# Performance work log

Measured on AMD Instinct MI355X. Metric: run time of the kernel, lower is better.

Reference implementation:

```python
import jax, jax.numpy as jnp
import numpy as np

B, NPTS = 2, 60000
NX, NY = 256, 256
PCR0, PCR1 = -32.0, -32.0
PS0, PS1 = 0.25, 0.25
MAXPP = 32      # max points per pillar
MAXP = 12000    # max pillars
C = 64          # lidar_channels
SENT = NX * NY  # sentinel pillar id (> any valid id)
NEG = -1e9
EPS = 1e-5


def setup_inputs():
    key = jax.random.key(0)
    ks = jax.random.split(key, 16)
    xy = jax.random.uniform(ks[0], (B, NPTS, 2), minval=-34.0, maxval=34.0)
    z = jax.random.uniform(ks[1], (B, NPTS, 1), minval=-3.0, maxval=1.0)
    ir = jax.random.uniform(ks[2], (B, NPTS, 2))
    pts = jnp.concatenate([xy, z, ir], axis=-1).astype(jnp.float32)
    mask = jax.random.uniform(ks[3], (B, NPTS)) < 0.98

    def lin(k, i, o):
        return (jax.random.normal(k, (i, o)) / np.sqrt(i)).astype(jnp.float32)

    inp = {"lidar_points": pts, "lidar_mask": mask,
           "w1": lin(ks[4], 10, 64), "b1": 0.01 * jax.random.normal(ks[5], (64,), jnp.float32),
           "g1": jnp.ones(64, jnp.float32), "be1": jnp.zeros(64, jnp.float32),
           "w2": lin(ks[6], 64, 64), "b2": 0.01 * jax.random.normal(ks[7], (64,), jnp.float32),
           "g2": jnp.ones(64, jnp.float32), "be2": jnp.zeros(64, jnp.float32)}
    for i, n in enumerate(["1", "2", "3"]):
        inp["cw" + n] = (jax.random.normal(ks[8 + i], (64, 64, 3, 3)) / np.sqrt(64 * 9)).astype(jnp.float32)
        inp["cb" + n] = 0.01 * jax.random.normal(ks[11 + i], (64,), jnp.float32)
        inp["cg" + n] = jnp.ones(64, jnp.float32)
        inp["cbe" + n] = jnp.zeros(64, jnp.float32)
    return inp


def bn1d(x, g, b):  # training-mode BN over rows (biased var), matches torch BatchNorm1d forward
    m = x.mean(0)
    v = ((x - m) ** 2).mean(0)
    return (x - m) * jax.lax.rsqrt(v + EPS) * g + b


def bn2d(x, g, b):  # training-mode BN over (N,H,W) per channel
    m = x.mean((0, 2, 3), keepdims=True)
    v = ((x - m) ** 2).mean((0, 2, 3), keepdims=True)
    return (x - m) * jax.lax.rsqrt(v + EPS) * g[None, :, None, None] + b[None, :, None, None]


def conv3(x, w, b):
    y = jax.lax.conv_general_dilated(x, w, (1, 1), 'SAME',
                                     dimension_numbers=('NCHW', 'OIHW', 'NCHW'))
    return y + b[None, :, None, None]


def pillarize(pts, msk):
    """pts: (N,5) xyzir, msk: (N,) bool -> padded pillar tensors (fixed shapes)."""
    n = pts.shape[0]
    ix = jnp.clip(((pts[:, 0] - PCR0) / PS0).astype(jnp.int32), 0, NX - 1)
    iy = jnp.clip(((pts[:, 1] - PCR1) / PS1).astype(jnp.int32), 0, NY - 1)
    pid = jnp.where(msk, iy * NX + ix, SENT)
    # sorted unique ids; keep the first (smallest) MAXP, like torch.unique + truncation
    spid = jnp.sort(pid)
    is_new = jnp.concatenate([jnp.array([True]), spid[1:] != spid[:-1]])
    urank = jnp.cumsum(is_new) - 1
    dest = jnp.where(is_new & (urank < MAXP) & (spid < SENT), urank, MAXP)
    uids = jnp.full((MAXP + 1,), SENT, dtype=pid.dtype).at[dest].set(spid)[:MAXP]  # ascending, SENT-padded
    inv = jnp.clip(jnp.searchsorted(uids, pid), 0, MAXP - 1)
    valid = (uids[inv] == pid) & (pid < SENT)
    # rank of each point within its pillar, in original point order (stable sort)
    seg = jnp.where(valid, inv, MAXP)
    order = jnp.argsort(seg)  # stable
    sseg = seg[order]
    pos = jnp.arange(n)
    first = jnp.concatenate([jnp.array([True]), sseg[1:] != sseg[:-1]])
    start = jax.lax.cummax(jnp.where(first, pos, 0))
    rank = jnp.zeros(n, jnp.int32).at[order].set((pos - start).astype(jnp.int32))
    keep = valid & (rank < MAXPP)  # first MAXPP points per pillar (matches truncation-then-mean)
    seg2 = jnp.where(keep, inv, MAXP)  # dump slot = MAXP
    cnt = jnp.zeros(MAXP + 1, pts.dtype).at[seg2].add(1.0)
    sums = jnp.zeros((MAXP + 1, 3), pts.dtype).at[seg2].add(jnp.where(keep[:, None], pts[:, :3], 0.0))
    mean = sums / jnp.maximum(cnt, 1.0)[:, None]
    ctr = mean[seg2]  # per-point pillar centroid (over kept points)
    gx = PCR0 + ((pid % NX).astype(pts.dtype) + 0.5) * PS0
    gy = PCR1 + ((pid // NX).astype(pts.dtype) + 0.5) * PS1
    aug = jnp.concatenate([pts, pts[:, :3] - ctr, gx[:, None], gy[:, None]], axis=1)  # (N,10)
    rk = jnp.minimum(rank, MAXPP - 1)
    pf = jnp.zeros((MAXP + 1, MAXPP, 10), pts.dtype).at[seg2, rk].set(
        jnp.where(keep[:, None], aug, 0.0))[:MAXP]
    pm = jnp.zeros((MAXP + 1, MAXPP), bool).at[seg2, rk].set(keep)[:MAXP]
    pvalid = uids < SENT
    coords = jnp.where(pvalid[:, None], jnp.stack([uids % NX, uids // NX], axis=-1), 0)
    return pf, pm, coords, pvalid


def pillar_net(pf, pm, w1, b1, g1, be1, w2, b2, g2, be2):
    npil, pp, ci = pf.shape
    x = pf.reshape(npil * pp, ci) @ w1 + b1
    x = jax.nn.relu(bn1d(x, g1, be1))
    x = x @ w2 + b2
    x = jax.nn.relu(bn1d(x, g2, be2))
    x = x.reshape(npil, pp, -1)
    x = jnp.where(pm[:, :, None], x, NEG)
    return x.max(axis=1)  # (npil, C)


def reference(lidar_points, lidar_mask, w1, b1, g1, be1, w2, b2, g2, be2,
              cw1, cb1, cg1, cbe1, cw2, cb2, cg2, cbe2, cw3, cb3, cg3, cbe3):
    pf, pm, coords, pvalid = jax.vmap(pillarize)(lidar_points, lidar_mask)
    # pillar net is applied per batch element in the original loop -> per-sample BN stats
    feat = jax.vmap(lambda a, m: pillar_net(a, m, w1, b1, g1, be1, w2, b2, g2, be2))(pf, pm)
    lin = coords[..., 1] * NX + coords[..., 0]          # (B, MAXP)
    f = jnp.where(pvalid[..., None], feat, 0.0)          # padded pillars contribute nothing
    bev = jax.vmap(lambda l, ff: jnp.zeros((NY * NX, C), ff.dtype).at[l].add(ff))(lin, f)
    bev = bev.reshape(-1, NY, NX, C).transpose(0, 3, 1, 2)  # (B,C,NY,NX)
    x = jax.nn.relu(bn2d(conv3(bev, cw1, cb1), cg1, cbe1))
    x = jax.nn.relu(bn2d(conv3(x, cw2, cb2), cg2, cbe2))
    x = jax.nn.relu(bn2d(conv3(x, cw3, cb3), cg3, cbe3))
    return x
```

## Files before the change

### kernel.cpp

```cpp
#include <hip/hip_runtime.h>

#define NPTS 60000
#define NXG 256
#define NCELL 65536
#define MAXP 12000
#define MAXPP 32
#define NROWS (MAXP*MAXPP)

typedef float f32x32 __attribute__((ext_vector_type(32)));
typedef float f32x4  __attribute__((ext_vector_type(4)));
typedef short s16x8  __attribute__((ext_vector_type(8)));

__device__ __forceinline__ short to_bf16(float f){
  unsigned u = __float_as_uint(f);
  unsigned r = (u + 0x7FFFu + ((u>>16)&1u)) >> 16;
  return (short)r;
}
__device__ __forceinline__ unsigned mapf(float f){
  unsigned u = __float_as_uint(f);
  return (u & 0x80000000u) ? ~u : (u | 0x80000000u);
}
__device__ __forceinline__ float unmapf(unsigned u){
  unsigned b = (u & 0x80000000u) ? (u ^ 0x80000000u) : ~u;
  return __uint_as_float(b);
}

__global__ __launch_bounds__(256) void prep(uint4* __restrict__ p1, size_t n1,
                                            uint4* __restrict__ p2, size_t n2,
                                            const float* __restrict__ w0, const float* __restrict__ w1,
                                            const float* __restrict__ w2, short* __restrict__ wh,
                                            const float* __restrict__ mw1, const float* __restrict__ mw2,
                                            short* __restrict__ w1h, short* __restrict__ w2h,
                                            uint4* __restrict__ fmn, size_t nfmn){
  size_t idx = (size_t)blockIdx.x*256 + threadIdx.x;
  size_t stride = (size_t)gridDim.x*256;
  const uint4 z = make_uint4(0,0,0,0);
  const uint4 ff = make_uint4(0xFFFFFFFFu,0xFFFFFFFFu,0xFFFFFFFFu,0xFFFFFFFFu);
  for (size_t k=idx; k<n1; k+=stride) p1[k]=z;
  for (size_t k=idx; k<n2; k+=stride) p2[k]=z;
  for (size_t k=idx; k<nfmn; k+=stride) fmn[k]=ff;
  for (size_t k=idx; k<3*36864; k+=stride){
    int l = (int)(k / 36864), r = (int)(k - (size_t)l*36864);
    const float* w = (l==0)? w0 : ((l==1)? w1 : w2);
    int ic = r & 63, oc = (r>>6)&63, tap = r>>12;
    wh[k] = to_bf16(w[(oc*64+ic)*9 + tap]);
  }
  for (size_t k=idx; k<2048; k+=stride){
    int kk = (int)(k>>6), oc = (int)(k&63);
    w1h[k] = (kk<10) ? to_bf16(mw1[kk*64+oc]) : (short)0;
  }
  for (size_t k=idx; k<4096; k+=stride)
    w2h[k] = to_bf16(mw2[k]);
}

__global__ void compute_pid(const float* __restrict__ pts, const void* __restrict__ maskp,
                            int* __restrict__ pid, int* __restrict__ pptr,
                            int* __restrict__ ccnt){
  __shared__ int cf32, cbig;
  if (threadIdx.x==0){ cf32=0; cbig=0; }
  __syncthreads();
  {
    int lf=0, lb=0;
    const unsigned* mu = (const unsigned*)maskp;
    for (int k=0;k<4;k++){
      unsigned x = mu[threadIdx.x*4+k];
      if (x==0x3f800000u) lf++;
      else if (x>1u) lb++;
    }
    if (lf) atomicAdd(&cf32, lf);
    if (lb) atomicAdd(&cbig, lb);
  }
  __syncthreads();
  int mode = (cf32>64) ? 2 : ((cbig>0) ? 1 : 0);
  int i = blockIdx.x*blockDim.x + threadIdx.x;
  if (i>=NPTS) return;
  int b = blockIdx.y;
  int gi = b*NPTS+i;
  bool m;
  if (mode==0)      m = ((const int*)maskp)[gi]!=0;
  else if (mode==1) m = ((const unsigned char*)maskp)[gi]!=0;
  else              m = ((const float*)maskp)[gi]!=0.f;
  int cell = -1;
  if (m){
    float x = pts[(size_t)gi*5+0], y = pts[(size_t)gi*5+1];
    int ix = (int)((x - (-32.0f)) / 0.25f);
    ix = ix<0?0:(ix>255?255:ix);
    int iy = (int)((y - (-32.0f)) / 0.25f);
    iy = iy<0?0:(iy>255?255:iy);
    cell = iy*NXG + ix;
    atomicAdd(&ccnt[b*NCELL+cell], 1);
  }
  pid[gi] = cell;
  pptr[gi] = -1;
}

__global__ __launch_bounds__(256) void scan_a(const int* __restrict__ ccnt,
                                              int2* __restrict__ bpart){
  int b = blockIdx.y, blk = blockIdx.x, t = threadIdx.x;
  int4 v = *(const int4*)&ccnt[b*NCELL + blk*1024 + t*4];
  int occ = (v.x>0)+(v.y>0)+(v.z>0)+(v.w>0);
  int cnt = v.x+v.y+v.z+v.w;
  #pragma unroll
  for (int off=32; off>0; off>>=1){
    occ += __shfl_xor(occ, off, 64);
    cnt += __shfl_xor(cnt, off, 64);
  }
  __shared__ int so[4], sc[4];
  int wv = t>>6, lane = t&63;
  if (lane==0){ so[wv]=occ; sc[wv]=cnt; }
  __syncthreads();
  if (t==0) bpart[b*64+blk] = make_int2(so[0]+so[1]+so[2]+so[3], sc[0]+sc[1]+sc[2]+sc[3]);
}

__global__ __launch_bounds__(256) void scan_b(const int* __restrict__ ccnt,
    const int2* __restrict__ bpart,
    int* __restrict__ crank, int* __restrict__ cstart, int* __restrict__ pcell,
    int* __restrict__ misc, int* __restrict__ heavy){
  __shared__ int swo[4], swc[4], sk[4];
  __shared__ int bo_, bc_;
  int b = blockIdx.y, blk = blockIdx.x, t = threadIdx.x;
  int wv = t>>6, lane = t&63;
  if (t < 64){
    int2 p = bpart[b*64+t];
    int po = (t<blk)? p.x : 0;
    int pc = (t<blk)? p.y : 0;
    int to = p.x;
    int tc = p.y;
    #pragma unroll
    for (int off=32; off>0; off>>=1){
      po += __shfl_xor(po, off, 64);
      pc += __shfl_xor(pc, off, 64);
      to += __shfl_xor(to, off, 64);
      tc += __shfl_xor(tc, off, 64);
    }
    if (t==0){
      bo_ = po; bc_ = pc;
      if (blk==0){
        misc[1+b] = (to < MAXP) ? to : MAXP;
        misc[5+b] = tc;
      }
    }
  }
  int4 v = *(const int4*)&ccnt[b*NCELL + blk*1024 + t*4];
  int occ = (v.x>0)+(v.y>0)+(v.z>0)+(v.w>0);
  int cnt = v.x+v.y+v.z+v.w;
  int io = occ, ic = cnt;
  #pragma unroll
  for (int off=1; off<64; off<<=1){
    int ao = __shfl_up(io, off, 64);
    int ac = __shfl_up(ic, off, 64);
    if (lane >= off){ io += ao; ic += ac; }
  }
  if (lane==63){ swo[wv]=io; swc[wv]=ic; }
  __syncthreads();
  int wvo=0, wvc=0;
  #pragma unroll
  for (int w2=0; w2<4; w2++){
    if (w2<wv){ wvo += swo[w2]; wvc += swc[w2]; }
  }
  int eo = bo_ + wvo + io - occ;
  int ec = bc_ + wvc + ic - cnt;
  int kept = 0;
  int cellb = blk*1024 + t*4;
  int vv[4] = {v.x,v.y,v.z,v.w};
  #pragma unroll
  for (int j=0;j<4;j++){
    int c = cellb+j; int val = vv[j];
    if (val>0){
      crank[b*NCELL+c]=eo; cstart[b*NCELL+c]=ec;
      if (eo<MAXP){
        pcell[b*MAXP+eo]=c;
        kept += (val<MAXPP)? val : MAXPP;
        if (val>MAXPP){
          int hi = atomicAdd(&heavy[b],1);
          if (hi<64) heavy[2 + b*64 + hi] = c;
        }
      }
      eo++; ec+=val;
    }
  }
  #pragma unroll
  for (int off=32; off>0; off>>=1) kept += __shfl_xor(kept, off, 64);
  if (lane==0) sk[wv]=kept;
  __syncthreads();
  if (t==0) atomicAdd(&misc[3+b], sk[0]+sk[1]+sk[2]+sk[3]);
}

__global__ void scatter_points(const int* __restrict__ pid, const int* __restrict__ ccnt,
    const int* __restrict__ crank, const int* __restrict__ cstart,
    int* __restrict__ ctmp, int* __restrict__ plist, int* __restrict__ pptr){
  int i = blockIdx.x*blockDim.x + threadIdx.x;
  if (i>=NPTS) return;
  int b = blockIdx.y;
  int gi = b*NPTS+i;
  int cell = pid[gi];
  if (cell<0) return;
  int bc = b*NCELL+cell;
  int pos = cstart[bc] + atomicAdd(&ctmp[bc],1);
  plist[b*NPTS+pos] = i;
  int r = crank[bc];
  if (r>=0 && r<MAXP && ccnt[bc]<=MAXPP) pptr[gi] = r;
}

__global__ void heavy_select(const int* __restrict__ ccnt, const int* __restrict__ crank,
    const int* __restrict__ cstart, const int* __restrict__ plist,
    const int* __restrict__ heavy, int* __restrict__ pptr){
  int b = blockIdx.y;
  int hn = heavy[b]; if (hn>64) hn=64;
  if ((int)blockIdx.x >= hn) return;
  int cell = heavy[2 + b*64 + blockIdx.x];
  int bc = b*NCELL+cell;
  int cnt = ccnt[bc], start = cstart[bc], pr = crank[bc];
  for (int e=threadIdx.x; e<cnt; e+=blockDim.x){
    int pe = plist[b*NPTS+start+e];
    int rank=0;
    for (int k=0;k<cnt;k++) rank += (plist[b*NPTS+start+k] < pe);
    if (rank<MAXPP) pptr[b*NPTS+pe] = pr;
  }
}

__global__ __launch_bounds__(256) void gather_cpts(const float* __restrict__ pts,
    const int* __restrict__ pid, const int* __restrict__ pptr,
    const int* __restrict__ plist, const int* __restrict__ misc,
    float* __restrict__ cpts, float* __restrict__ psum){
  int pos = blockIdx.x*256 + threadIdx.x;
  int b = blockIdx.y;
  if (pos >= misc[5+b]) return;
  int i = plist[b*NPTS+pos];
  int gi = b*NPTS+i;
  const float* qp = &pts[(size_t)gi*5];
  float x=qp[0], y=qp[1], z=qp[2], i1=qp[3], i2=qp[4];
  int cell = pid[gi];
  int rid = pptr[gi];
  float gx = -32.0f + ((float)(cell&255)+0.5f)*0.25f;
  float gy = -32.0f + ((float)(cell>>8)+0.5f)*0.25f;
  float4* cp = (float4*)&cpts[(size_t)(b*NPTS+pos)*12];
  cp[0] = make_float4(x,y,z,i1);
  cp[1] = make_float4(i2,gx,gy,__int_as_float(rid));
  if (rid>=0){
    float* s = &psum[(size_t)(b*MAXP+rid)*4];
    atomicAdd(s+0,x); atomicAdd(s+1,y); atomicAdd(s+2,z); atomicAdd(s+3,1.f);
  }
}

#define MM_ACC(K,V) { if ((K)<32) m0[(K)&31]+=(V); else if ((K)<64) m1[((K)-32)&31]+=(V); else m2+=(V); }
__global__ __launch_bounds__(256) void moments(float* __restrict__ cpts,
    const float* __restrict__ psum, const int* __restrict__ misc,
    float* __restrict__ lstat){
  int b = blockIdx.y;
  int n = misc[5+b];
  f32x32 m0, m1; float m2 = 0.f;
  #pragma unroll
  for (int j=0;j<32;j++){ m0[j]=0.f; m1[j]=0.f; }
  for (int pos = blockIdx.x*256+threadIdx.x; pos<n; pos += gridDim.x*256){
    float4* cp = (float4*)&cpts[(size_t)(b*NPTS+pos)*12];
    float4 f1 = cp[0], f2 = cp[1];
    int rid = __float_as_int(f2.w);
    if (rid<0) continue;
    float4 mc = *(const float4*)&psum[(size_t)(b*MAXP+rid)*4];
    float inv = 1.f/fmaxf(mc.w,1.f);
    float dx = f1.x-mc.x*inv, dy = f1.y-mc.y*inv, dz = f1.z-mc.z*inv;
    cp[2] = make_float4(dx,dy,dz,0.f);
    float aug[10] = {f1.x,f1.y,f1.z,f1.w,f2.x, dx,dy,dz, f2.y,f2.z};
    #pragma unroll
    for (int d=0; d<10; d++){
      #pragma unroll
      for (int e=d; e<10; e++){
        const int k = d*10 - d*(d-1)/2 + (e-d);
        MM_ACC(k, aug[d]*aug[e]);
      }
      const int kl = 55+d;
      MM_ACC(kl, aug[d]);
    }
  }
  int lane = threadIdx.x & 63;
  int rep = ((blockIdx.x*256+threadIdx.x)>>6) & 15;
  float* dst = &lstat[(size_t)(rep*2+b)*65];
  #pragma unroll
  for (int j=0;j<32;j++){
    float v = m0[j];
    #pragma unroll
    for (int off=32; off>0; off>>=1) v += __shfl_xor(v, off, 64);
    if (lane==0) atomicAdd(&dst[j], v);
  }
  #pragma unroll
  for (int j=0;j<32;j++){
    float v = m1[j];
    #pragma unroll
    for (int off=32; off>0; off>>=1) v += __shfl_xor(v, off, 64);
    if (lane==0) atomicAdd(&dst[32+j], v);
  }
  {
    float v = m2;
    #pragma unroll
    for (int off=32; off>0; off>>=1) v += __shfl_xor(v, off, 64);
    if (lane==0) atomicAdd(&dst[64], v);
  }
}

#define MFMA16(A,B,C) __builtin_amdgcn_mfma_f32_16x16x32_bf16(A,B,C,0,0,0)

__global__ __launch_bounds__(256) void point_mlp(const float* __restrict__ cpts,
    const int* __restrict__ misc,
    const float* __restrict__ w1, const float* __restrict__ b1,
    const float* __restrict__ g1, const float* __restrict__ be1,
    const short* __restrict__ w1h, const short* __restrict__ w2h,
    const float* __restrict__ lstat, float* __restrict__ tbuf){
  __shared__ float sM[65];
  __shared__ float sBN1[128];
  __shared__ short zT[4][16*72];
  const int b = blockIdx.y;
  const int t = threadIdx.x;
  for (int e=t; e<65; e+=256){
    float s=0.f;
    for (int r=0;r<16;r++) s += lstat[(size_t)(r*2+b)*65+e];
    sM[e]=s;
  }
  __syncthreads();
  if (t < 64){
    int c = t;
    float wcol[10];
    #pragma unroll
    for (int d=0;d<10;d++) wcol[d] = w1[d*64+c];
    float b1c = b1[c];
    float nk = (float)misc[3+b];
    const float N = (float)NROWS;
    float pad = N - nk;
    float lw = 0.f;
    #pragma unroll
    for (int d=0;d<10;d++) lw += sM[55+d]*wcol[d];
    float s = nk*b1c + lw;
    float qq = nk*b1c*b1c + 2.f*b1c*lw;
    #pragma unroll
    for (int d=0; d<10; d++){
      #pragma unroll
      for (int e=d; e<10; e++){
        float m = sM[d*10 - d*(d-1)/2 + (e-d)];
        qq += ((d==e)?1.f:2.f)*m*wcol[d]*wcol[e];
      }
    }
    float St = s + pad*b1c;
    float Qt = qq + pad*b1c*b1c;
    float mu = St/N;
    float var = fmaxf(Qt/N - mu*mu, 0.f);
    float sc = g1[c]*rsqrtf(var+1e-5f);
    float sh = be1[c]-mu*sc;
    sBN1[c]=sc; sBN1[64+c]=b1c*sc+sh;
  }
  __syncthreads();
  const int lane = t & 63, wv = t >> 6;
  const int colx = lane & 15;
  const int kq = lane >> 4, kb = kq*8;
  s16x8 w1f0, w1f1, w1f2, w1f3;
  s16x8 a2f0, a2f1, a2f2, a2f3;
  s16x8 b2f0, b2f1, b2f2, b2f3;
  #pragma unroll
  for (int j=0;j<8;j++){
    w1f0[j]=w1h[(kb+j)*64 +  0+colx]; w1f1[j]=w1h[(kb+j)*64 + 16+colx];
    w1f2[j]=w1h[(kb+j)*64 + 32+colx]; w1f3[j]=w1h[(kb+j)*64 + 48+colx];
    a2f0[j]=w2h[(kb+j)*64 +  0+colx]; a2f1[j]=w2h[(kb+j)*64 + 16+colx];
    a2f2[j]=w2h[(kb+j)*64 + 32+colx]; a2f3[j]=w2h[(kb+j)*64 + 48+colx];
    b2f0[j]=w2h[(32+kb+j)*64 +  0+colx]; b2f1[j]=w2h[(32+kb+j)*64 + 16+colx];
    b2f2[j]=w2h[(32+kb+j)*64 + 32+colx]; b2f3[j]=w2h[(32+kb+j)*64 + 48+colx];
  }
  float sc1v0=sBN1[colx],    sh1v0=sBN1[64+colx];
  float sc1v1=sBN1[16+colx], sh1v1=sBN1[80+colx];
  float sc1v2=sBN1[32+colx], sh1v2=sBN1[96+colx];
  float sc1v3=sBN1[48+colx], sh1v3=sBN1[112+colx];
  const int n = misc[5+b];
  const int ntiles = (n+15)>>4;
  short* myZ = zT[wv];
  for (int tile = blockIdx.x*4 + wv; tile < ntiles; tile += gridDim.x*4){
    int pos0 = tile*16;
    int pos = pos0 + colx;
    float aug[10];
    #pragma unroll
    for (int d=0;d<10;d++) aug[d]=0.f;
    if (pos < n){
      const float4* cp = (const float4*)&cpts[(size_t)(b*NPTS+pos)*12];
      float4 f1 = cp[0], f2 = cp[1], f3 = cp[2];
      aug[0]=f1.x; aug[1]=f1.y; aug[2]=f1.z; aug[3]=f1.w; aug[4]=f2.x;
      aug[5]=f3.x; aug[6]=f3.y; aug[7]=f3.z;
      aug[8]=f2.y; aug[9]=f2.z;
    }
    s16x8 af;
    #pragma unroll
    for (int j=0;j<8;j++){
      float v = 0.f;
      if (kq==0) v = aug[j];
      else if (kq==1 && j<2) v = aug[8+j];
      af[j] = to_bf16(v);
    }
    f32x4 y0={0.f,0.f,0.f,0.f}, y1=y0, y2=y0, y3=y0;
    y0 = MFMA16(af, w1f0, y0);
    y1 = MFMA16(af, w1f1, y1);
    y2 = MFMA16(af, w1f2, y2);
    y3 = MFMA16(af, w1f3, y3);
    #pragma unroll
    for (int m=0;m<4;m++){
      int pr = (kq*4+m)*72;
      myZ[pr +  0+colx] = to_bf16(fmaxf(y0[m]*sc1v0+sh1v0, 0.f));
      myZ[pr + 16+colx] = to_bf16(fmaxf(y1[m]*sc1v1+sh1v1, 0.f));
      myZ[pr + 32+colx] = to_bf16(fmaxf(y2[m]*sc1v2+sh1v2, 0.f));
      myZ[pr + 48+colx] = to_bf16(fmaxf(y3[m]*sc1v3+sh1v3, 0.f));
    }
    s16x8 az0 = *(const s16x8*)&myZ[colx*72 + kb];
    s16x8 az1 = *(const s16x8*)&myZ[colx*72 + 32 + kb];
    f32x4 t0={0.f,0.f,0.f,0.f}, t1=t0, t2=t0, t3=t0;
    t0 = MFMA16(az0, a2f0, t0); t0 = MFMA16(az1, b2f0, t0);
    t1 = MFMA16(az0, a2f1, t1); t1 = MFMA16(az1, b2f1, t1);
    t2 = MFMA16(az0, a2f2, t2); t2 = MFMA16(az1, b2f2, t2);
    t3 = MFMA16(az0, a2f3, t3); t3 = MFMA16(az1, b2f3, t3);
    #pragma unroll
    for (int m=0;m<4;m++){
      int pm = pos0 + kq*4 + m;
      if (pm < n){
        float* dst = &tbuf[(size_t)(b*NPTS+pm)*64];
        dst[ 0+colx] = t0[m];
        dst[16+colx] = t1[m];
        dst[32+colx] = t2[m];
        dst[48+colx] = t3[m];
      }
    }
  }
}

__global__ __launch_bounds__(256) void seg_max(const float* __restrict__ tbuf,
    const float* __restrict__ cpts, const int* __restrict__ misc,
    float* __restrict__ l2stat, unsigned* __restrict__ fmxU, unsigned* __restrict__ fmnU){
  const int b = blockIdx.y;
  const int lane = threadIdx.x & 63;
  const int n = misc[5+b];
  const int w = blockIdx.x*4 + (threadIdx.x>>6);
  float s2 = 0.f, q2 = 0.f;
  int p0 = w*16;
  if (p0 < n){
    int p1 = p0+16; if (p1>n) p1=n;
    int cur = -1;
    float tmax = -1e30f, tmin = 1e30f;
    for (int pos=p0; pos<p1; ++pos){
      int rid = __float_as_int(cpts[(size_t)(b*NPTS+pos)*12 + 7]);
      float tv = tbuf[(size_t)(b*NPTS+pos)*64 + lane];
      if (rid >= 0){
        if (rid != cur){
          if (cur >= 0){
            atomicMax(&fmxU[(size_t)(b*MAXP+cur)*64 + lane], mapf(tmax));
            atomicMin(&fmnU[(size_t)(b*MAXP+cur)*64 + lane], mapf(tmin));
          }
          cur = rid; tmax = -1e30f; tmin = 1e30f;
        }
        tmax = fmaxf(tmax, tv);
        tmin = fminf(tmin, tv);
        s2 += tv; q2 += tv*tv;
      }
    }
    if (cur >= 0){
      atomicMax(&fmxU[(size_t)(b*MAXP+cur)*64 + lane], mapf(tmax));
      atomicMin(&fmnU[(size_t)(b*MAXP+cur)*64 + lane], mapf(tmin));
    }
  }
  int rep = w & 15;
  atomicAdd(&l2stat[((rep*2+b)*2+0)*64+lane], s2);
  atomicAdd(&l2stat[((rep*2+b)*2+1)*64+lane], q2);
}

__global__ void stats_fin2(const float* __restrict__ w1, const float* __restrict__ b1,
    const float* __restrict__ g1, const float* __restrict__ be1,
    const float* __restrict__ w2, const float* __restrict__ b2,
    const float* __restrict__ g2, const float* __restrict__ be2,
    const float* __restrict__ lstat, const float* __restrict__ l2stat,
    const int* __restrict__ misc, float* __restrict__ stats){
  __shared__ float M[65];
  __shared__ float z0s[64];
  int b = blockIdx.x, c = threadIdx.x;
  for (int e=c; e<65; e+=64){
    float s=0.f;
    for (int r=0;r<16;r++) s += lstat[(size_t)(r*2+b)*65+e];
    M[e]=s;
  }
  __syncthreads();
  float wcol[10];
  #pragma unroll
  for (int d=0;d<10;d++) wcol[d] = w1[d*64+c];
  float b1c = b1[c];
  float nk = (float)misc[3+b];
  const float N = (float)NROWS;
  float pad = N - nk;
  float lw = 0.f;
  #pragma unroll
  for (int d=0;d<10;d++) lw += M[55+d]*wcol[d];
  float s = nk*b1c + lw;
  float qq = nk*b1c*b1c + 2.f*b1c*lw;
  #pragma unroll
  for (int d=0; d<10; d++){
    #pragma unroll
    for (int e=d; e<10; e++){
      float m = M[d*10 - d*(d-1)/2 + (e-d)];
      qq += ((d==e)?1.f:2.f)*m*wcol[d]*wcol[e];
    }
  }
  float St = s + pad*b1c;
  float Qt = qq + pad*b1c*b1c;
  float mu = St/N;
  float var = fmaxf(Qt/N - mu*mu, 0.f);
  float sc1 = g1[c]*rsqrtf(var+1e-5f);
  float sh1 = be1[c]-mu*sc1;
  float z0 = fmaxf(b1c*sc1+sh1, 0.f);
  z0s[c]=z0;
  __syncthreads();
  float t0 = b2[c];
  for (int i2=0;i2<64;i2++) t0 += z0s[i2]*w2[(size_t)i2*64+c];
  float s2 = pad*t0, q2 = pad*t0*t0;
  for (int r=0;r<16;r++){
    s2 += l2stat[((r*2+b)*2+0)*64+c];
    q2 += l2stat[((r*2+b)*2+1)*64+c];
  }
  float m2 = s2/N;
  float v2 = fmaxf(q2/N - m2*m2, 0.f);
  float sc2 = g2[c]*rsqrtf(v2+1e-5f);
  float* S = &stats[(size_t)b*512];
  S[384+c]=sc2; S[448+c]=be2[c]-m2*sc2;
}

__global__ void scatter_bev(const unsigned* __restrict__ fmxU, const unsigned* __restrict__ fmnU,
                            const int* __restrict__ pcell, const int* __restrict__ misc,
                            const float* __restrict__ stats, short* __restrict__ bevh){
  int tid = blockIdx.x*256+threadIdx.x;
  if (tid >= 2*64*MAXP) return;
  int c = tid & 63;
  int bp = tid >> 6;
  int b = bp / MAXP;
  int p = bp - b*MAXP;
  if (p >= misc[1+b]) return;
  float sc2 = stats[(size_t)b*512+384+c], sh2 = stats[(size_t)b*512+448+c];
  float t = (sc2 >= 0.f) ? unmapf(fmxU[tid]) : unmapf(fmnU[tid]);
  float v = fmaxf(sc2*t+sh2, 0.f);
  int cell = pcell[b*MAXP+p];
  bevh[((size_t)((b<<16) + cell))*64 + c] = to_bf16(v);
}

__global__ __launch_bounds__(512,4) void conv_mfma(const short* __restrict__ xh,
    const short* __restrict__ wh, const float* __restrict__ bias,
    const float* __restrict__ pstat, const float* __restrict__ pg, const float* __restrict__ pbe,
    short* __restrict__ outh, float* __restrict__ outf,
    float* __restrict__ stat){
  __shared__ short sX[324*40];
  __shared__ short sW[576*40];
  __shared__ float sBN[128];
  __shared__ float ss[64], sq[64];
  const int tX = blockIdx.x*16, tY = blockIdx.y*16;
  const int b = blockIdx.z;
  const int t = threadIdx.x;
  const int lane = t & 63, wv = t >> 6;
  const int colx = lane & 15;
  const int kb = (lane >> 4) * 8;
  const int ocb = (wv >> 2) * 32;
  const int ry  = (wv & 3) * 4;
  if (t < 64){ ss[t]=0.f; sq[t]=0.f; }
  if (t >= 64 && t < 128 && pstat){
    int c = t-64;
    const float n = 131072.f;
    float m = pstat[c]/n;
    float v = fmaxf(pstat[64+c]/n - m*m, 0.f);
    float sc = pg[c]*rsqrtf(v+1e-5f);
    sBN[c]=sc; sBN[64+c]=pbe[c]-m*sc;
  }

  f32x4 a00={0.f,0.f,0.f,0.f}, a01=a00, a02=a00, a03=a00;
  f32x4 a10=a00, a11=a00, a12=a00, a13=a00;

  for (int h=0; h<2; ++h){
    __syncthreads();
    for (int e=t; e<1296; e+=512){
      int px = e>>2, j = e&3;
      int yy = px/18, xx = px - yy*18;
      int gy = tY+yy-1, gx = tX+xx-1;
      uint4 v = make_uint4(0,0,0,0);
      if ((unsigned)gy<256u && (unsigned)gx<256u){
        v = *(const uint4*)&xh[((size_t)((b<<16) + (gy<<8) + gx))*64 + h*32 + j*8];
        if (pstat){
          unsigned arr[4] = {v.x, v.y, v.z, v.w};
          #pragma unroll
          for (int j2=0;j2<4;j2++){
            unsigned wrd = arr[j2];
            int ch = h*32 + j*8 + j2*2;
            float lo = __uint_as_float(wrd<<16);
            float hi = __uint_as_float(wrd & 0xffff0000u);
            lo = fmaxf(lo*sBN[ch]+sBN[64+ch], 0.f);
            hi = fmaxf(hi*sBN[ch+1]+sBN[64+ch+1], 0.f);
            arr[j2] = (unsigned)(unsigned short)to_bf16(lo) |
                      (((unsigned)(unsigned short)to_bf16(hi))<<16);
          }
          v = make_uint4(arr[0],arr[1],arr[2],arr[3]);
        }
      }
      *(uint4*)&sX[px*40 + j*8] = v;
    }
    for (int e=t; e<2304; e+=512){
      int row = e>>2, j = e&3;
      int tap = row>>6, oc = row&63;
      uint4 v = *(const uint4*)&wh[(size_t)tap*4096 + oc*64 + h*32 + j*8];
      *(uint4*)&sW[row*40 + j*8] = v;
    }
    __syncthreads();
    #pragma unroll
    for (int tap=0; tap<9; ++tap){
      const int dy = tap/3, dx = tap - dy*3;
      s16x8 wA = *(const s16x8*)&sW[(tap*64 + ocb +  0 + colx)*40 + kb];
      s16x8 wB = *(const s16x8*)&sW[(tap*64 + ocb + 16 + colx)*40 + kb];
      s16x8 x0 = *(const s16x8*)&sX[((ry+0+dy)*18 + colx+dx)*40 + kb];
      s16x8 x1 = *(const s16x8*)&sX[((ry+1+dy)*18 + colx+dx)*40 + kb];
      s16x8 x2 = *(const s16x8*)&sX[((ry+2+dy)*18 + colx+dx)*40 + kb];
      s16x8 x3 = *(const s16x8*)&sX[((ry+3+dy)*18 + colx+dx)*40 + kb];
      a00 = MFMA16(wA,x0,a00); a01 = MFMA16(wA,x1,a01);
      a02 = MFMA16(wA,x2,a02); a03 = MFMA16(wA,x3,a03);
      a10 = MFMA16(wB,x0,a10); a11 = MFMA16(wB,x1,a11);
      a12 = MFMA16(wB,x2,a12); a13 = MFMA16(wB,x3,a13);
    }
  }
  const int ocl = (lane>>4)*4;
  #define DOG(G, A0,A1,A2,A3) { \
    const int oc0g = ocb + G*16 + ocl; \
    float bj0=bias[oc0g], bj1=bias[oc0g+1], bj2=bias[oc0g+2], bj3=bias[oc0g+3]; \
    float v00=A0[0]+bj0, v01=A0[1]+bj1, v02=A0[2]+bj2, v03=A0[3]+bj3; \
    float v10=A1[0]+bj0, v11=A1[1]+bj1, v12=A1[2]+bj2, v13=A1[3]+bj3; \
    float v20=A2[0]+bj0, v21=A2[1]+bj1, v22=A2[2]+bj2, v23=A2[3]+bj3; \
    float v30=A3[0]+bj0, v31=A3[1]+bj1, v32=A3[2]+bj2, v33=A3[3]+bj3; \
    float s0=v00+v10+v20+v30, q0=v00*v00+v10*v10+v20*v20+v30*v30; \
    float s1=v01+v11+v21+v31, q1=v01*v01+v11*v11+v21*v21+v31*v31; \
    float s2=v02+v12+v22+v32, q2=v02*v02+v12*v12+v22*v22+v32*v32; \
    float s3=v03+v13+v23+v33, q3=v03*v03+v13*v13+v23*v23+v33*v33; \
    s0+=__shfl_xor(s0,1,64); s0+=__shfl_xor(s0,2,64); s0+=__shfl_xor(s0,4,64); s0+=__shfl_xor(s0,8,64); \
    q0+=__shfl_xor(q0,1,64); q0+=__shfl_xor(q0,2,64); q0+=__shfl_xor(q0,4,64); q0+=__shfl_xor(q0,8,64); \
    s1+=__shfl_xor(s1,1,64); s1+=__shfl_xor(s1,2,64); s1+=__shfl_xor(s1,4,64); s1+=__shfl_xor(s1,8,64); \
    q1+=__shfl_xor(q1,1,64); q1+=__shfl_xor(q1,2,64); q1+=__shfl_xor(q1,4,64); q1+=__shfl_xor(q1,8,64); \
    s2+=__shfl_xor(s2,1,64); s2+=__shfl_xor(s2,2,64); s2+=__shfl_xor(s2,4,64); s2+=__shfl_xor(s2,8,64); \
    q2+=__shfl_xor(q2,1,64); q2+=__shfl_xor(q2,2,64); q2+=__shfl_xor(q2,4,64); q2+=__shfl_xor(q2,8,64); \
    s3+=__shfl_xor(s3,1,64); s3+=__shfl_xor(s3,2,64); s3+=__shfl_xor(s3,4,64); s3+=__shfl_xor(s3,8,64); \
    q3+=__shfl_xor(q3,1,64); q3+=__shfl_xor(q3,2,64); q3+=__shfl_xor(q3,4,64); q3+=__shfl_xor(q3,8,64); \
    if (colx==0){ \
      atomicAdd(&ss[oc0g],s0);   atomicAdd(&sq[oc0g],q0); \
      atomicAdd(&ss[oc0g+1],s1); atomicAdd(&sq[oc0g+1],q1); \
      atomicAdd(&ss[oc0g+2],s2); atomicAdd(&sq[oc0g+2],q2); \
      atomicAdd(&ss[oc0g+3],s3); atomicAdd(&sq[oc0g+3],q3); \
    } \
    if (outh){ \
      size_t pb = (size_t)((b<<16) + tX + colx); \
      *(short4*)&outh[(pb + ((tY+ry+0)<<8))*64 + oc0g] = make_short4(to_bf16(v00),to_bf16(v01),to_bf16(v02),to_bf16(v03)); \
      *(short4*)&outh[(pb + ((tY+ry+1)<<8))*64 + oc0g] = make_short4(to_bf16(v10),to_bf16(v11),to_bf16(v12),to_bf16(v13)); \
      *(short4*)&outh[(pb + ((tY+ry+2)<<8))*64 + oc0g] = make_short4(to_bf16(v20),to_bf16(v21),to_bf16(v22),to_bf16(v23)); \
      *(short4*)&outh[(pb + ((tY+ry+3)<<8))*64 + oc0g] = make_short4(to_bf16(v30),to_bf16(v31),to_bf16(v32),to_bf16(v33)); \
    } else { \
      size_t cb0 = (((size_t)(b*64+oc0g))<<16) + ((tY+ry)<<8) + tX + colx; \
      outf[cb0          ] = v00; outf[cb0+(1<<16)      ] = v01; outf[cb0+(2<<16)      ] = v02; outf[cb0+(3<<16)      ] = v03; \
      outf[cb0+256      ] = v10; outf[cb0+(1<<16)+256  ] = v11; outf[cb0+(2<<16)+256  ] = v12; outf[cb0+(3<<16)+256  ] = v13; \
      outf[cb0+512      ] = v20; outf[cb0+(1<<16)+512  ] = v21; outf[cb0+(2<<16)+512  ] = v22; outf[cb0+(3<<16)+512  ] = v23; \
      outf[cb0+768      ] = v30; outf[cb0+(1<<16)+768  ] = v31; outf[cb0+(2<<16)+768  ] = v32; outf[cb0+(3<<16)+768  ] = v33; \
    } \
  }
  DOG(0, a00,a01,a02,a03)
  DOG(1, a10,a11,a12,a13)
  #undef DOG
  __syncthreads();
  if (t < 64){
    atomicAdd(&stat[t],    ss[t]);
    atomicAdd(&stat[64+t], sq[t]);
  }
}

__global__ __launch_bounds__(256) void bn_apply(float* __restrict__ x, const float* __restrict__ bnst,
                                                const float* __restrict__ g, const float* __restrict__ be){
  __shared__ float sBN[128];
  if (threadIdx.x < 64){
    int c = threadIdx.x;
    const float n = 131072.f;
    float m = bnst[c]/n;
    float v = fmaxf(bnst[64+c]/n - m*m, 0.f);
    float sc = g[c]*rsqrtf(v+1e-5f);
    sBN[c]=sc; sBN[64+c]=be[c]-m*sc;
  }
  __syncthreads();
  size_t idx = (size_t)blockIdx.x*256 + threadIdx.x;
  size_t stride = (size_t)gridDim.x*256;
  float4* p = (float4*)x;
  for (size_t k=idx; k<2097152ULL; k+=stride){
    int c = (int)((k>>14)&63);
    float sc = sBN[c], sh = sBN[64+c];
    float4 v = p[k];
    v.x=fmaxf(v.x*sc+sh,0.f); v.y=fmaxf(v.y*sc+sh,0.f);
    v.z=fmaxf(v.z*sc+sh,0.f); v.w=fmaxf(v.w*sc+sh,0.f);
    p[k]=v;
  }
}

extern "C" void kernel_launch(void* const* d_in, const int* in_sizes, int n_in,
                              void* d_out, int out_size, void* d_ws, size_t ws_size,
                              hipStream_t stream){
  const float* pts  = (const float*)d_in[0];
  const void*  mask = d_in[1];
  const float* w1 = (const float*)d_in[2];
  const float* b1 = (const float*)d_in[3];
  const float* g1 = (const float*)d_in[4];
  const float* be1= (const float*)d_in[5];
  const float* w2 = (const float*)d_in[6];
  const float* b2 = (const float*)d_in[7];
  const float* g2 = (const float*)d_in[8];
  const float* be2= (const float*)d_in[9];
  const float* cw[3]  = {(const float*)d_in[10],(const float*)d_in[14],(const float*)d_in[18]};
  const float* cb[3]  = {(const float*)d_in[11],(const float*)d_in[15],(const float*)d_in[19]};
  const float* cg[3]  = {(const float*)d_in[12],(const float*)d_in[16],(const float*)d_in[20]};
  const float* cbe[3] = {(const float*)d_in[13],(const float*)d_in[17],(const float*)d_in[21]};
  float* out = (float*)d_out;

  char* W = (char*)d_ws;
  size_t off = 0;
  auto A = [&](size_t n){ size_t r = off; off = (off + n + 255) & ~(size_t)255; return r; };
  short*    BIGH  = (short*)   (W + A((size_t)2*NCELL*64*2));
  short*    OUT1H = (short*)   (W + A((size_t)2*NCELL*64*2));
  int*      PID   = (int*)     (W + A((size_t)2*NPTS*4));
  int*      CRANK = (int*)     (W + A((size_t)2*NCELL*4));
  int*      CSTART= (int*)     (W + A((size_t)2*NCELL*4));
  int*      PLIST = (int*)     (W + A((size_t)2*NPTS*4));
  int*      PPTR  = (int*)     (W + A((size_t)2*NPTS*4));
  int*      PCELL = (int*)     (W + A((size_t)2*MAXP*4));
  float*    CPTS  = (float*)   (W + A((size_t)2*NPTS*12*4));
  float*    TBUF  = (float*)   (W + A((size_t)2*NPTS*64*4));
  unsigned* FMN   = (unsigned*)(W + A((size_t)2*MAXP*64*4));
  short*    WH    = (short*)   (W + A((size_t)3*36864*2));
  short*    W1H   = (short*)   (W + A((size_t)2048*2));
  short*    W2H   = (short*)   (W + A((size_t)4096*2));
  int2*     BPART = (int2*)    (W + A((size_t)2*64*8));
  size_t zbeg = off;
  unsigned* FMX   = (unsigned*)(W + A((size_t)2*MAXP*64*4));
  int*      CCNT  = (int*)     (W + A((size_t)2*NCELL*4));
  int*      CTMP  = (int*)     (W + A((size_t)2*NCELL*4));
  float*    PSUM  = (float*)   (W + A((size_t)2*MAXP*16));
  float*    STATS = (float*)   (W + A((size_t)2*512*4));
  float*    LSTAT = (float*)   (W + A((size_t)16*2*65*4));
  float*    L2STAT= (float*)   (W + A((size_t)16*2*2*64*4));
  float*    BNST  = (float*)   (W + A((size_t)3*256*4));
  int*      HEAVY = (int*)     (W + A((size_t)(2+2*64)*4));
  int*      MISC  = (int*)     (W + A(256));
  size_t zend = off;

  prep<<<2048,256,0,stream>>>((uint4*)BIGH, (size_t)2*NCELL*64*2/16,
                              (uint4*)(W+zbeg), (zend-zbeg)/16,
                              cw[0], cw[1], cw[2], WH, w1, w2, W1H, W2H,
                              (uint4*)FMN, (size_t)2*MAXP*64*4/16);

  dim3 perPt((NPTS+255)/256, 2);

  compute_pid<<<perPt,256,0,stream>>>(pts, mask, PID, PPTR, CCNT);
  scan_a<<<dim3(64,2),256,0,stream>>>(CCNT, BPART);
  scan_b<<<dim3(64,2),256,0,stream>>>(CCNT, BPART, CRANK, CSTART, PCELL, MISC, HEAVY);
  scatter_points<<<perPt,256,0,stream>>>(PID, CCNT, CRANK, CSTART, CTMP, PLIST, PPTR);
  heavy_select<<<dim3(64,2),64,0,stream>>>(CCNT, CRANK, CSTART, PLIST, HEAVY, PPTR);
  gather_cpts<<<perPt,256,0,stream>>>(pts, PID, PPTR, PLIST, MISC, CPTS, PSUM);
  moments<<<dim3(120,2),256,0,stream>>>(CPTS, PSUM, MISC, LSTAT);
  point_mlp<<<dim3(256,2),256,0,stream>>>(CPTS, MISC, w1, b1, g1, be1,
                                          W1H, W2H, LSTAT, TBUF);
  seg_max<<<dim3(938,2),256,0,stream>>>(TBUF, CPTS, MISC, L2STAT, FMX, FMN);
  stats_fin2<<<2,64,0,stream>>>(w1, b1, g1, be1, w2, b2, g2, be2, LSTAT, L2STAT, MISC, STATS);
  scatter_bev<<<(2*64*MAXP+255)/256,256,0,stream>>>(FMX, FMN, PCELL, MISC, STATS, BIGH);

  conv_mfma<<<dim3(16,16,2),512,0,stream>>>(BIGH, WH, cb[0], nullptr, nullptr, nullptr,
                                            OUT1H, nullptr, BNST);
  conv_mfma<<<dim3(16,16,2),512,0,stream>>>(OUT1H, WH+36864, cb[1], BNST, cg[0], cbe[0],
                                            BIGH, nullptr, BNST+256);
  conv_mfma<<<dim3(16,16,2),512,0,stream>>>(BIGH, WH+2*36864, cb[2], BNST+256, cg[1], cbe[1],
                                            nullptr, out, BNST+512);
  bn_apply<<<2048,256,0,stream>>>(out, BNST+512, cg[2], cbe[2]);
}
```

Measured before the change: 216.2 us.

## Fuse pillar-point pipeline: scatter+gather, MLP+segmax, stats+BEV scatter

Merges scatter_points and gather_cpts so compacted point records and pillar sums are written directly at scatter time, with heavy_select patching the rid and sums for overflowed cells. point_mlp now does the per-pillar segmented max/min and the second-layer BN sums itself, so the 64-wide per-point TBUF intermediate is never written or re-read. stats_fin2 is folded into scatter_bev, with each block recomputing the BN2 scale and shift redundantly. This removes several launches and a large global round-trip. The cost is more atomics inside the MFMA kernel and redundant per-block stats computation.

```diff
diff --git a/kernel.cpp b/kernel.cpp
--- a/kernel.cpp
+++ b/kernel.cpp
@@ -54,8 +54,7 @@
 }
 
 __global__ void compute_pid(const float* __restrict__ pts, const void* __restrict__ maskp,
-                            int* __restrict__ pid, int* __restrict__ pptr,
-                            int* __restrict__ ccnt){
+                            int* __restrict__ pid, int* __restrict__ ccnt){
   __shared__ int cf32, cbig;
   if (threadIdx.x==0){ cf32=0; cbig=0; }
   __syncthreads();
@@ -91,7 +90,6 @@
     atomicAdd(&ccnt[b*NCELL+cell], 1);
   }
   pid[gi] = cell;
-  pptr[gi] = -1;
 }
 
 __global__ __launch_bounds__(256) void scan_a(const int* __restrict__ ccnt,
@@ -186,9 +184,10 @@
   if (t==0) atomicAdd(&misc[3+b], sk[0]+sk[1]+sk[2]+sk[3]);
 }
 
-__global__ void scatter_points(const int* __restrict__ pid, const int* __restrict__ ccnt,
-    const int* __restrict__ crank, const int* __restrict__ cstart,
-    int* __restrict__ ctmp, int* __restrict__ plist, int* __restrict__ pptr){
+__global__ void scatter_cpts(const float* __restrict__ pts, const int* __restrict__ pid,
+    const int* __restrict__ ccnt, const int* __restrict__ crank, const int* __restrict__ cstart,
+    int* __restrict__ ctmp, int* __restrict__ plist,
+    float* __restrict__ cpts, float* __restrict__ psum){
   int i = blockIdx.x*blockDim.x + threadIdx.x;
   if (i>=NPTS) return;
   int b = blockIdx.y;
@@ -198,13 +197,25 @@
   int bc = b*NCELL+cell;
   int pos = cstart[bc] + atomicAdd(&ctmp[bc],1);
   plist[b*NPTS+pos] = i;
-  int r = crank[bc];
-  if (r>=0 && r<MAXP && ccnt[bc]<=MAXPP) pptr[gi] = r;
-}
-
-__global__ void heavy_select(const int* __restrict__ ccnt, const int* __restrict__ crank,
+  int cnt = ccnt[bc], r = crank[bc];
+  int rid = (r<MAXP && cnt<=MAXPP) ? r : -1;
+  const float* qp = &pts[(size_t)gi*5];
+  float x=qp[0], y=qp[1], z=qp[2], i1=qp[3], i2=qp[4];
+  float gx = -32.0f + ((float)(cell&255)+0.5f)*0.25f;
+  float gy = -32.0f + ((float)(cell>>8)+0.5f)*0.25f;
+  float4* cp = (float4*)&cpts[(size_t)(b*NPTS+pos)*12];
+  cp[0] = make_float4(x,y,z,i1);
+  cp[1] = make_float4(i2,gx,gy,__int_as_float(rid));
+  if (rid>=0){
+    float* s = &psum[(size_t)(b*MAXP+rid)*4];
+    atomicAdd(s+0,x); atomicAdd(s+1,y); atomicAdd(s+2,z); atomicAdd(s+3,1.f);
+  }
+}
+
+__global__ void heavy_select(const float* __restrict__ pts,
+    const int* __restrict__ ccnt, const int* __restrict__ crank,
     const int* __restrict__ cstart, const int* __restrict__ plist,
-    const int* __restrict__ heavy, int* __restrict__ pptr){
+    const int* __restrict__ heavy, float* __restrict__ cpts, float* __restrict__ psum){
   int b = blockIdx.y;
   int hn = heavy[b]; if (hn>64) hn=64;
   if ((int)blockIdx.x >= hn) return;
@@ -215,31 +226,12 @@
     int pe = plist[b*NPTS+start+e];
     int rank=0;
     for (int k=0;k<cnt;k++) rank += (plist[b*NPTS+start+k] < pe);
-    if (rank<MAXPP) pptr[b*NPTS+pe] = pr;
-  }
-}
-
-__global__ __launch_bounds__(256) void gather_cpts(const float* __restrict__ pts,
-    const int* __restrict__ pid, const int* __restrict__ pptr,
-    const int* __restrict__ plist, const int* __restrict__ misc,
-    float* __restrict__ cpts, float* __restrict__ psum){
-  int pos = blockIdx.x*256 + threadIdx.x;
-  int b = blockIdx.y;
-  if (pos >= misc[5+b]) return;
-  int i = plist[b*NPTS+pos];
-  int gi = b*NPTS+i;
-  const float* qp = &pts[(size_t)gi*5];
-  float x=qp[0], y=qp[1], z=qp[2], i1=qp[3], i2=qp[4];
-  int cell = pid[gi];
-  int rid = pptr[gi];
-  float gx = -32.0f + ((float)(cell&255)+0.5f)*0.25f;
-  float gy = -32.0f + ((float)(cell>>8)+0.5f)*0.25f;
-  float4* cp = (float4*)&cpts[(size_t)(b*NPTS+pos)*12];
-  cp[0] = make_float4(x,y,z,i1);
-  cp[1] = make_float4(i2,gx,gy,__int_as_float(rid));
-  if (rid>=0){
-    float* s = &psum[(size_t)(b*MAXP+rid)*4];
-    atomicAdd(s+0,x); atomicAdd(s+1,y); atomicAdd(s+2,z); atomicAdd(s+3,1.f);
+    if (rank<MAXPP && pr<MAXP){
+      cpts[(size_t)(b*NPTS+start+e)*12 + 7] = __int_as_float(pr);
+      const float* qp = &pts[(size_t)(b*NPTS+pe)*5];
+      float* s = &psum[(size_t)(b*MAXP+pr)*4];
+      atomicAdd(s+0,qp[0]); atomicAdd(s+1,qp[1]); atomicAdd(s+2,qp[2]); atomicAdd(s+3,1.f);
+    }
   }
 }
 
@@ -305,7 +297,8 @@
     const float* __restrict__ w1, const float* __restrict__ b1,
     const float* __restrict__ g1, const float* __restrict__ be1,
     const short* __restrict__ w1h, const short* __restrict__ w2h,
-    const float* __restrict__ lstat, float* __restrict__ tbuf){
+    const float* __restrict__ lstat, float* __restrict__ l2stat,
+    unsigned* __restrict__ fmxU, unsigned* __restrict__ fmnU){
   __shared__ float sM[65];
   __shared__ float sBN1[128];
   __shared__ short zT[4][16*72];
@@ -370,6 +363,7 @@
   const int n = misc[5+b];
   const int ntiles = (n+15)>>4;
   short* myZ = zT[wv];
+  f32x4 s24={0.f,0.f,0.f,0.f}, q24=s24;
   for (int tile = blockIdx.x*4 + wv; tile < ntiles; tile += gridDim.x*4){
     int pos0 = tile*16;
     int pos = pos0 + colx;
@@ -411,132 +405,146 @@
     t1 = MFMA16(az0, a2f1, t1); t1 = MFMA16(az1, b2f1, t1);
     t2 = MFMA16(az0, a2f2, t2); t2 = MFMA16(az1, b2f2, t2);
     t3 = MFMA16(az0, a2f3, t3); t3 = MFMA16(az1, b2f3, t3);
+    int cur = -1;
+    f32x4 tmx={-1e30f,-1e30f,-1e30f,-1e30f}, tmn={1e30f,1e30f,1e30f,1e30f};
     #pragma unroll
     for (int m=0;m<4;m++){
       int pm = pos0 + kq*4 + m;
-      if (pm < n){
-        float* dst = &tbuf[(size_t)(b*NPTS+pm)*64];
-        dst[ 0+colx] = t0[m];
-        dst[16+colx] = t1[m];
-        dst[32+colx] = t2[m];
-        dst[48+colx] = t3[m];
+      int rid = -1;
+      if (pm < n) rid = __float_as_int(cpts[(size_t)(b*NPTS+pm)*12 + 7]);
+      if (rid != cur){
+        if (cur >= 0){
+          size_t base = (size_t)(b*MAXP+cur)*64;
+          atomicMax(&fmxU[base+ 0+colx], mapf(tmx[0]));
+          atomicMax(&fmxU[base+16+colx], mapf(tmx[1]));
+          atomicMax(&fmxU[base+32+colx], mapf(tmx[2]));
+          atomicMax(&fmxU[base+48+colx], mapf(tmx[3]));
+          atomicMin(&fmnU[base+ 0+colx], mapf(tmn[0]));
+          atomicMin(&fmnU[base+16+colx], mapf(tmn[1]));
+          atomicMin(&fmnU[base+32+colx], mapf(tmn[2]));
+          atomicMin(&fmnU[base+48+colx], mapf(tmn[3]));
+        }
+        cur = rid;
+        tmx[0]=-1e30f; tmx[1]=-1e30f; tmx[2]=-1e30f; tmx[3]=-1e30f;
+        tmn[0]= 1e30f; tmn[1]= 1e30f; tmn[2]= 1e30f; tmn[3]= 1e30f;
       }
-    }
-  }
-}
-
-__global__ __launch_bounds__(256) void seg_max(const float* __restrict__ tbuf,
-    const float* __restrict__ cpts, const int* __restrict__ misc,
-    float* __restrict__ l2stat, unsigned* __restrict__ fmxU, unsigned* __restrict__ fmnU){
-  const int b = blockIdx.y;
-  const int lane = threadIdx.x & 63;
-  const int n = misc[5+b];
-  const int w = blockIdx.x*4 + (threadIdx.x>>6);
-  float s2 = 0.f, q2 = 0.f;
-  int p0 = w*16;
-  if (p0 < n){
-    int p1 = p0+16; if (p1>n) p1=n;
-    int cur = -1;
-    float tmax = -1e30f, tmin = 1e30f;
-    for (int pos=p0; pos<p1; ++pos){
-      int rid = __float_as_int(cpts[(size_t)(b*NPTS+pos)*12 + 7]);
-      float tv = tbuf[(size_t)(b*NPTS+pos)*64 + lane];
       if (rid >= 0){
-        if (rid != cur){
-          if (cur >= 0){
-            atomicMax(&fmxU[(size_t)(b*MAXP+cur)*64 + lane], mapf(tmax));
-            atomicMin(&fmnU[(size_t)(b*MAXP+cur)*64 + lane], mapf(tmin));
-          }
-          cur = rid; tmax = -1e30f; tmin = 1e30f;
-        }
-        tmax = fmaxf(tmax, tv);
-        tmin = fminf(tmin, tv);
-        s2 += tv; q2 += tv*tv;
+        float v0=t0[m], v1=t1[m], v2=t2[m], v3=t3[m];
+        tmx[0]=fmaxf(tmx[0],v0); tmn[0]=fminf(tmn[0],v0);
+        tmx[1]=fmaxf(tmx[1],v1); tmn[1]=fminf(tmn[1],v1);
+        tmx[2]=fmaxf(tmx[2],v2); tmn[2]=fminf(tmn[2],v2);
+        tmx[3]=fmaxf(tmx[3],v3); tmn[3]=fminf(tmn[3],v3);
+        s24[0]+=v0; q24[0]+=v0*v0;
+        s24[1]+=v1; q24[1]+=v1*v1;
+        s24[2]+=v2; q24[2]+=v2*v2;
+        s24[3]+=v3; q24[3]+=v3*v3;
       }
     }
     if (cur >= 0){
-      atomicMax(&fmxU[(size_t)(b*MAXP+cur)*64 + lane], mapf(tmax));
-      atomicMin(&fmnU[(size_t)(b*MAXP+cur)*64 + lane], mapf(tmin));
-    }
-  }
-  int rep = w & 15;
-  atomicAdd(&l2stat[((rep*2+b)*2+0)*64+lane], s2);
-  atomicAdd(&l2stat[((rep*2+b)*2+1)*64+lane], q2);
-}
-
-__global__ void stats_fin2(const float* __restrict__ w1, const float* __restrict__ b1,
+      size_t base = (size_t)(b*MAXP+cur)*64;
+      atomicMax(&fmxU[base+ 0+colx], mapf(tmx[0]));
+      atomicMax(&fmxU[base+16+colx], mapf(tmx[1]));
+      atomicMax(&fmxU[base+32+colx], mapf(tmx[2]));
+      atomicMax(&fmxU[base+48+colx], mapf(tmx[3]));
+      atomicMin(&fmnU[base+ 0+colx], mapf(tmn[0]));
+      atomicMin(&fmnU[base+16+colx], mapf(tmn[1]));
+      atomicMin(&fmnU[base+32+colx], mapf(tmn[2]));
+      atomicMin(&fmnU[base+48+colx], mapf(tmn[3]));
+    }
+  }
+  int rep = (blockIdx.x*4 + wv) & 15;
+  float* L = &l2stat[(size_t)((rep*2+b)*2+0)*64];
+  atomicAdd(&L[ 0+colx], s24[0]);
+  atomicAdd(&L[16+colx], s24[1]);
+  atomicAdd(&L[32+colx], s24[2]);
+  atomicAdd(&L[48+colx], s24[3]);
+  float* Q = &l2stat[(size_t)((rep*2+b)*2+1)*64];
+  atomicAdd(&Q[ 0+colx], q24[0]);
+  atomicAdd(&Q[16+colx], q24[1]);
+  atomicAdd(&Q[32+colx], q24[2]);
+  atomicAdd(&Q[48+colx], q24[3]);
+}
+
+__global__ __launch_bounds__(256) void scatter_bev(
+    const float* __restrict__ w1, const float* __restrict__ b1,
     const float* __restrict__ g1, const float* __restrict__ be1,
     const float* __restrict__ w2, const float* __restrict__ b2,
     const float* __restrict__ g2, const float* __restrict__ be2,
     const float* __restrict__ lstat, const float* __restrict__ l2stat,
-    const int* __restrict__ misc, float* __restrict__ stats){
+    const unsigned* __restrict__ fmxU, const unsigned* __restrict__ fmnU,
+    const int* __restrict__ pcell, const int* __restrict__ misc,
+    short* __restrict__ bevh){
   __shared__ float M[65];
   __shared__ float z0s[64];
-  int b = blockIdx.x, c = threadIdx.x;
-  for (int e=c; e<65; e+=64){
+  __shared__ float sBN2[128];
+  const int b = blockIdx.y;
+  for (int e=threadIdx.x; e<65; e+=256){
     float s=0.f;
     for (int r=0;r<16;r++) s += lstat[(size_t)(r*2+b)*65+e];
     M[e]=s;
   }
   __syncthreads();
-  float wcol[10];
-  #pragma unroll
-  for (int d=0;d<10;d++) wcol[d] = w1[d*64+c];
-  float b1c = b1[c];
-  float nk = (float)misc[3+b];
-  const float N = (float)NROWS;
-  float pad = N - nk;
-  float lw = 0.f;
-  #pragma unroll
-  for (int d=0;d<10;d++) lw += M[55+d]*wcol[d];
-  float s = nk*b1c + lw;
-  float qq = nk*b1c*b1c + 2.f*b1c*lw;
-  #pragma unroll
-  for (int d=0; d<10; d++){
-    #pragma unroll
-    for (int e=d; e<10; e++){
-      float m = M[d*10 - d*(d-1)/2 + (e-d)];
-      qq += ((d==e)?1.f:2.f)*m*wcol[d]*wcol[e];
-    }
-  }
-  float St = s + pad*b1c;
-  float Qt = qq + pad*b1c*b1c;
-  float mu = St/N;
-  float var = fmaxf(Qt/N - mu*mu, 0.f);
-  float sc1 = g1[c]*rsqrtf(var+1e-5f);
-  float sh1 = be1[c]-mu*sc1;
-  float z0 = fmaxf(b1c*sc1+sh1, 0.f);
-  z0s[c]=z0;
-  __syncthreads();
-  float t0 = b2[c];
-  for (int i2=0;i2<64;i2++) t0 += z0s[i2]*w2[(size_t)i2*64+c];
-  float s2 = pad*t0, q2 = pad*t0*t0;
-  for (int r=0;r<16;r++){
-    s2 += l2stat[((r*2+b)*2+0)*64+c];
-    q2 += l2stat[((r*2+b)*2+1)*64+c];
-  }
-  float m2 = s2/N;
-  float v2 = fmaxf(q2/N - m2*m2, 0.f);
-  float sc2 = g2[c]*rsqrtf(v2+1e-5f);
-  float* S = &stats[(size_t)b*512];
-  S[384+c]=sc2; S[448+c]=be2[c]-m2*sc2;
-}
-
-__global__ void scatter_bev(const unsigned* __restrict__ fmxU, const unsigned* __restrict__ fmnU,
-                            const int* __restrict__ pcell, const int* __restrict__ misc,
-                            const float* __restrict__ stats, short* __restrict__ bevh){
-  int tid = blockIdx.x*256+threadIdx.x;
-  if (tid >= 2*64*MAXP) return;
-  int c = tid & 63;
-  int bp = tid >> 6;
-  int b = bp / MAXP;
-  int p = bp - b*MAXP;
-  if (p >= misc[1+b]) return;
-  float sc2 = stats[(size_t)b*512+384+c], sh2 = stats[(size_t)b*512+448+c];
-  float t = (sc2 >= 0.f) ? unmapf(fmxU[tid]) : unmapf(fmnU[tid]);
-  float v = fmaxf(sc2*t+sh2, 0.f);
-  int cell = pcell[b*MAXP+p];
-  bevh[((size_t)((b<<16) + cell))*64 + c] = to_bf16(v);
+  if (threadIdx.x < 64){
+    int c = threadIdx.x;
+    float wcol[10];
+    #pragma unroll
+    for (int d=0;d<10;d++) wcol[d] = w1[d*64+c];
+    float b1c = b1[c];
+    float nk = (float)misc[3+b];
+    const float N = (float)NROWS;
+    float pad = N - nk;
+    float lw = 0.f;
+    #pragma unroll
+    for (int d=0;d<10;d++) lw += M[55+d]*wcol[d];
+    float s = nk*b1c + lw;
+    float qq = nk*b1c*b1c + 2.f*b1c*lw;
+    #pragma unroll
+    for (int d=0; d<10; d++){
+      #pragma unroll
+      for (int e=d; e<10; e++){
+        float m = M[d*10 - d*(d-1)/2 + (e-d)];
+        qq += ((d==e)?1.f:2.f)*m*wcol[d]*wcol[e];
+      }
+    }
+    float St = s + pad*b1c;
+    float Qt = qq + pad*b1c*b1c;
+    float mu = St/N;
+    float var = fmaxf(Qt/N - mu*mu, 0.f);
+    float sc1 = g1[c]*rsqrtf(var+1e-5f);
+    float sh1 = be1[c]-mu*sc1;
+    z0s[c] = fmaxf(b1c*sc1+sh1, 0.f);
+  }
+  __syncthreads();
+  if (threadIdx.x < 64){
+    int c = threadIdx.x;
+    float nk = (float)misc[3+b];
+    const float N = (float)NROWS;
+    float pad = N - nk;
+    float t0 = b2[c];
+    for (int i2=0;i2<64;i2++) t0 += z0s[i2]*w2[(size_t)i2*64+c];
+    float s2 = pad*t0, q2 = pad*t0*t0;
+    for (int r=0;r<16;r++){
+      s2 += l2stat[(size_t)((r*2+b)*2+0)*64+c];
+      q2 += l2stat[(size_t)((r*2+b)*2+1)*64+c];
+    }
+    float m2 = s2/N;
+    float v2 = fmaxf(q2/N - m2*m2, 0.f);
+    float sc2 = g2[c]*rsqrtf(v2+1e-5f);
+    sBN2[c]=sc2; sBN2[64+c]=be2[c]-m2*sc2;
+  }
+  __syncthreads();
+  const int npil = misc[1+b];
+  for (int tid = blockIdx.x*256+threadIdx.x; tid < 64*MAXP; tid += gridDim.x*256){
+    int c = tid & 63;
+    int p = tid >> 6;
+    if (p >= npil) break;
+    float sc2 = sBN2[c], sh2 = sBN2[64+c];
+    size_t idx = (size_t)(b*MAXP+p)*64 + c;
+    float tv = (sc2 >= 0.f) ? unmapf(fmxU[idx]) : unmapf(fmnU[idx]);
+    float v = fmaxf(sc2*tv+sh2, 0.f);
+    int cell = pcell[b*MAXP+p];
+    bevh[((size_t)((b<<16) + cell))*64 + c] = to_bf16(v);
+  }
 }
 
 __global__ __launch_bounds__(512,4) void conv_mfma(const short* __restrict__ xh,
@@ -721,10 +729,8 @@
   int*      CRANK = (int*)     (W + A((size_t)2*NCELL*4));
   int*      CSTART= (int*)     (W + A((size_t)2*NCELL*4));
   int*      PLIST = (int*)     (W + A((size_t)2*NPTS*4));
-  int*      PPTR  = (int*)     (W + A((size_t)2*NPTS*4));
   int*      PCELL = (int*)     (W + A((size_t)2*MAXP*4));
   float*    CPTS  = (float*)   (W + A((size_t)2*NPTS*12*4));
-  float*    TBUF  = (float*)   (W + A((size_t)2*NPTS*64*4));
   unsigned* FMN   = (unsigned*)(W + A((size_t)2*MAXP*64*4));
   short*    WH    = (short*)   (W + A((size_t)3*36864*2));
   short*    W1H   = (short*)   (W + A((size_t)2048*2));
@@ -735,7 +741,6 @@
   int*      CCNT  = (int*)     (W + A((size_t)2*NCELL*4));
   int*      CTMP  = (int*)     (W + A((size_t)2*NCELL*4));
   float*    PSUM  = (float*)   (W + A((size_t)2*MAXP*16));
-  float*    STATS = (float*)   (W + A((size_t)2*512*4));
   float*    LSTAT = (float*)   (W + A((size_t)16*2*65*4));
   float*    L2STAT= (float*)   (W + A((size_t)16*2*2*64*4));
   float*    BNST  = (float*)   (W + A((size_t)3*256*4));
@@ -750,18 +755,16 @@
 
   dim3 perPt((NPTS+255)/256, 2);
 
-  compute_pid<<<perPt,256,0,stream>>>(pts, mask, PID, PPTR, CCNT);
+  compute_pid<<<perPt,256,0,stream>>>(pts, mask, PID, CCNT);
   scan_a<<<dim3(64,2),256,0,stream>>>(CCNT, BPART);
   scan_b<<<dim3(64,2),256,0,stream>>>(CCNT, BPART, CRANK, CSTART, PCELL, MISC, HEAVY);
-  scatter_points<<<perPt,256,0,stream>>>(PID, CCNT, CRANK, CSTART, CTMP, PLIST, PPTR);
-  heavy_select<<<dim3(64,2),64,0,stream>>>(CCNT, CRANK, CSTART, PLIST, HEAVY, PPTR);
-  gather_cpts<<<perPt,256,0,stream>>>(pts, PID, PPTR, PLIST, MISC, CPTS, PSUM);
+  scatter_cpts<<<perPt,256,0,stream>>>(pts, PID, CCNT, CRANK, CSTART, CTMP, PLIST, CPTS, PSUM);
+  heavy_select<<<dim3(64,2),64,0,stream>>>(pts, CCNT, CRANK, CSTART, PLIST, HEAVY, CPTS, PSUM);
   moments<<<dim3(120,2),256,0,stream>>>(CPTS, PSUM, MISC, LSTAT);
   point_mlp<<<dim3(256,2),256,0,stream>>>(CPTS, MISC, w1, b1, g1, be1,
-                                          W1H, W2H, LSTAT, TBUF);
-  seg_max<<<dim3(938,2),256,0,stream>>>(TBUF, CPTS, MISC, L2STAT, FMX, FMN);
-  stats_fin2<<<2,64,0,stream>>>(w1, b1, g1, be1, w2, b2, g2, be2, LSTAT, L2STAT, MISC, STATS);
-  scatter_bev<<<(2*64*MAXP+255)/256,256,0,stream>>>(FMX, FMN, PCELL, MISC, STATS, BIGH);
+                                          W1H, W2H, LSTAT, L2STAT, FMX, FMN);
+  scatter_bev<<<dim3(512,2),256,0,stream>>>(w1, b1, g1, be1, w2, b2, g2, be2,
+                                            LSTAT, L2STAT, FMX, FMN, PCELL, MISC, BIGH);
 
   conv_mfma<<<dim3(16,16,2),512,0,stream>>>(BIGH, WH, cb[0], nullptr, nullptr, nullptr,
                                             OUT1H, nullptr, BNST);
```

Result: slower. 226.6 us (+4.8%).
